# Optimization experiments

Measured on AMD Instinct MI355X. Metric: run time of the kernel, lower is better.

## Reference

```python
import jax, jax.numpy as jnp
import numpy as np

# Module hyperparameters (from init_kwargs)
P = 96                 # num_of_patches
W = 1536.0             # input width
H = 1536.0             # input height
XPS = W / P            # x patch size = 16
YPS = H / P            # y patch size = 16
PROB_THR = 0.9
IOU_THR = 0.5
N = P * P              # total candidate boxes


def setup_inputs() -> dict:
    key = jax.random.key(0)
    # x: [5, P, P] -> channel 0 = probability, 1..4 = (x, y, w, h) in [0,1)
    x = jax.random.uniform(key, (5, P, P), dtype=jnp.float32)
    return {"x": x}


def _pairwise_iou(b):
    # b: [N, 4] xyxy
    x1, y1, x2, y2 = b[:, 0], b[:, 1], b[:, 2], b[:, 3]
    area = (x2 - x1) * (y2 - y1)                       # [N]
    ix1 = jnp.maximum(x1[:, None], x1[None, :])
    iy1 = jnp.maximum(y1[:, None], y1[None, :])
    ix2 = jnp.minimum(x2[:, None], x2[None, :])
    iy2 = jnp.minimum(y2[:, None], y2[None, :])
    inter = jnp.clip(ix2 - ix1, 0.0) * jnp.clip(iy2 - iy1, 0.0)
    union = area[:, None] + area[None, :] - inter
    return jnp.where(union > 0, inter / union, 0.0)    # [N, N]


def _forward(x):
    # --- scale_batch_bbx_xywh, applied densely (invalid entries are masked later) ---
    p = x[0]
    ii = jnp.arange(P, dtype=x.dtype)[:, None]   # row index i
    jj = jnp.arange(P, dtype=x.dtype)[None, :]   # col index j
    bx = x[1] * XPS + ii * XPS
    by = x[2] * YPS + jj * YPS
    bw = x[3] * W
    bh = x[4] * H
    bbx = jnp.stack([p, bx, by, bw, bh], axis=0).reshape(5, N).T   # [N, 5] (p, x, y, w, h)

    # --- remove_low_probability_bbx: fixed-shape validity mask instead of filtering ---
    scores = bbx[:, 0]
    valid = scores > PROB_THR

    # --- convert_batch_to_xyxy + round ---
    x1 = jnp.round(bbx[:, 1])
    y1 = jnp.round(bbx[:, 2])
    x2 = jnp.round(bbx[:, 3] + bbx[:, 1])
    y2 = jnp.round(bbx[:, 4] + bbx[:, 2])

    # --- greedy NMS (torchvision semantics): sort by score desc, suppress by IoU ---
    sort_key = jnp.where(valid, scores, -jnp.inf)
    order = jnp.argsort(-sort_key)
    boxes = jnp.stack([x1, y1, x2, y2], axis=1)[order]   # [N, 4] sorted
    sc = scores[order]
    v = valid[order]
    iou = _pairwise_iou(boxes)                           # [N, N]

    def body(kept, i):
        suppressed = jnp.any(kept & (iou[i] > IOU_THR))
        ki = v[i] & ~suppressed
        return kept.at[i].set(ki), ki

    _, keeps = jax.lax.scan(body, jnp.zeros((N,), bool), jnp.arange(N))

    # --- cat([scores, bbx]) then convert_batch_to_xywh on kept rows ---
    out = jnp.stack(
        [sc, boxes[:, 0], boxes[:, 1], boxes[:, 2] - boxes[:, 0], boxes[:, 3] - boxes[:, 1]],
        axis=1,
    )  # [N, 5] = (score, x, y, w, h), score-descending order like nms output
    out = jnp.where(keeps[:, None], out, 0.0)
    return out, keeps


def reference(x):
    # Returns (out [N,5], keep_mask [N]); rows with keep_mask=False are zeroed.
    # This is the fixed-shape equivalent of the variable-length torch output.
    return _forward(x)
```

## Files before the change

### kernel.cpp

```cpp
#include <hip/hip_runtime.h>

#define PP 96
#define NB (PP*PP)
#define NCH (NB/64)
#define PROB_THR 0.9f
#define FAST_CAP 1024
#define LSTRIDE 1034

typedef unsigned long long u64;
typedef unsigned int u32;

__device__ __forceinline__ void decode_core(int n, float xv, float yv, float wv, float hv,
                                            float& X1, float& Y1, float& X2, float& Y2)
{
    int i = n / PP;
    int j = n - i * PP;
    float bx = __fadd_rn(__fmul_rn(xv, 16.0f), (float)i * 16.0f);
    float by = __fadd_rn(__fmul_rn(yv, 16.0f), (float)j * 16.0f);
    float bw = __fmul_rn(wv, 1536.0f);
    float bh = __fmul_rn(hv, 1536.0f);
    X1 = rintf(bx);
    Y1 = rintf(by);
    X2 = rintf(__fadd_rn(bw, bx));
    Y2 = rintf(__fadd_rn(bh, by));
}

__device__ __forceinline__ void decode_box(const float* __restrict__ x, int n,
                                           float& X1, float& Y1, float& X2, float& Y2)
{
    decode_core(n, x[NB + n], x[2 * NB + n], x[3 * NB + n], x[4 * NB + n], X1, Y1, X2, Y2);
}

__device__ __forceinline__ int iou_hit_nodiv(float ix1, float iy1, float ix2, float iy2, float iar,
                                             float jx1, float jy1, float jx2, float jy2, float jar)
{
    float xx1 = fmaxf(ix1, jx1), yy1 = fmaxf(iy1, jy1);
    float xx2 = fminf(ix2, jx2), yy2 = fminf(iy2, jy2);
    float iw = fmaxf(__fsub_rn(xx2, xx1), 0.0f);
    float ih = fmaxf(__fsub_rn(yy2, yy1), 0.0f);
    float inter = __fmul_rn(iw, ih);
    float uni = __fsub_rn(__fadd_rn(iar, jar), inter);
    return (uni > 0.0f && __fadd_rn(inter, inter) > uni) ? 1 : 0;
}

__device__ __forceinline__ int iou_hit_div(float ix1, float iy1, float ix2, float iy2, float iar,
                                           float jx1, float jy1, float jx2, float jy2, float jar)
{
    float xx1 = fmaxf(ix1, jx1), yy1 = fmaxf(iy1, jy1);
    float xx2 = fminf(ix2, jx2), yy2 = fminf(iy2, jy2);
    float iw = fmaxf(__fsub_rn(xx2, xx1), 0.0f);
    float ih = fmaxf(__fsub_rn(yy2, yy1), 0.0f);
    float inter = __fmul_rn(iw, ih);
    float uni = __fsub_rn(__fadd_rn(iar, jar), inter);
    return (uni > 0.0f && __fdiv_rn(inter, uni) > 0.5f) ? 1 : 0;
}

__global__ void __launch_bounds__(256) k_sort(
    const float* __restrict__ x,
    float* __restrict__ gss, float4* __restrict__ gbox,
    u64* __restrict__ skeys, int* __restrict__ counter, int ws_ok)
{
    __shared__ u64 lmask[NCH];
    __shared__ int pc[NCH], loff[NCH];
    __shared__ int sM;
    __shared__ u64 kdb[FAST_CAP];
    __shared__ int prank[256];

    const int tid = threadIdx.x;
    const int lane = tid & 63;
    const int wv = tid >> 6;
    const int b = blockIdx.x;

    #pragma unroll
    for (int g = 0; g < 36; g += 6) {
        float sv[6];
        #pragma unroll
        for (int u = 0; u < 6; ++u)
            sv[u] = x[((wv * 36 + g + u) << 6) + lane];
        #pragma unroll
        for (int u = 0; u < 6; ++u) {
            u64 m = __ballot(sv[u] > PROB_THR);
            if (lane == 0) lmask[wv * 36 + g + u] = m;
        }
    }
    __syncthreads();
    if (tid < NCH) pc[tid] = __popcll(lmask[tid]);
    __syncthreads();
    if (tid < 64) {
        int acc = 0;
        for (int seg = 0; seg < 3; ++seg) {
            int c = (seg << 6) + lane;
            int pv = (c < NCH) ? pc[c] : 0;
            int v = pv;
            #pragma unroll
            for (int off = 1; off < 64; off <<= 1) {
                int u = __shfl_up(v, off);
                if (lane >= off) v += u;
            }
            if (c < NCH) loff[c] = acc + v - pv;
            acc += __shfl(v, 63);
        }
        if (lane == 0) sM = acc;
    }
    __syncthreads();
    const int M = sM;
    const bool fast = (M <= FAST_CAP) && ws_ok;
    if (b == 0 && tid == 0) counter[0] = M;

    if (!fast) {
        if (b == 0) {
            for (int c = wv; c < NCH; c += 4) {
                float s = x[(c << 6) + lane];
                u64 m = lmask[c];
                if ((m >> lane) & 1ull) {
                    int pos = loff[c] + __popcll(m & ((1ull << lane) - 1ull));
                    int n = (c << 6) + lane;
                    skeys[pos] = ((u64)__float_as_uint(s) << 32) | (u64)(NB - 1 - n);
                }
            }
        }
        return;
    }

    for (int c = wv; c < NCH; c += 4) {
        float s = x[(c << 6) + lane];
        u64 m = lmask[c];
        if ((m >> lane) & 1ull) {
            int pos = loff[c] + __popcll(m & ((1ull << lane) - 1ull));
            int n = (c << 6) + lane;
            kdb[pos] = ((u64)__float_as_uint(s) << 32) | (u64)(NB - 1 - n);
        }
    }
    for (int q = M + tid; q < FAST_CAP; q += 256) kdb[q] = 0ull;
    __syncthreads();

    const int cand = (b << 6) + lane;
    const u64 k0 = kdb[cand];
    const int n0 = NB - 1 - (int)(k0 & 0xFFFFFFFFull);
    float xv0 = x[NB + n0], yv0 = x[2 * NB + n0];
    float wv0 = x[3 * NB + n0], hv0 = x[4 * NB + n0];
    int r = 0;
    const int nck = (M + 63) >> 6;
    for (int ch = wv; ch < nck; ch += 4) {
        u64 kq = kdb[(ch << 6) + lane];
        u32 qlo = (u32)kq, qhi = (u32)(kq >> 32);
        #pragma unroll
        for (int i = 0; i < 64; ++i) {
            u32 blo = (u32)__builtin_amdgcn_readlane((int)qlo, i);
            u32 bhi = (u32)__builtin_amdgcn_readlane((int)qhi, i);
            u64 kb = ((u64)bhi << 32) | (u64)blo;
            r += (kb > k0) ? 1 : 0;
        }
    }
    prank[tid] = r;
    __syncthreads();
    if (tid < 64 && cand < M) {
        int rk = prank[tid] + prank[64 + tid] + prank[128 + tid] + prank[192 + tid];
        float X1, Y1, X2, Y2;
        decode_core(n0, xv0, yv0, wv0, hv0, X1, Y1, X2, Y2);
        gbox[rk] = make_float4(X1, Y1, X2, Y2);
        gss[rk] = __uint_as_float((u32)(k0 >> 32));
    }
}

__global__ void __launch_bounds__(256) k_adj(
    float* __restrict__ out, const float4* __restrict__ gbox,
    const int* __restrict__ counter, u64* __restrict__ adjT, int ws_ok)
{
    __shared__ float4 lb[FAST_CAP];
    __shared__ float la[FAST_CAP];
    int M = counter[0]; if (M > NB) M = NB;
    const int tid = threadIdx.x, lane = tid & 63, wv = tid >> 6, b = blockIdx.x;

    float4 z4 = make_float4(0.f, 0.f, 0.f, 0.f);
    for (int q = tid; q < 216; q += 256)
        ((float4*)out)[b * 216 + q] = z4;

    const bool fast = (M <= FAST_CAP) && ws_ok;
    if (!fast) return;
    if ((b << 4) >= M) return;

    const int W = (M + 63) >> 6;
    for (int f = tid; f < M; f += 256) {
        float4 bb = gbox[f];
        lb[f] = bb;
        la[f] = __fmul_rn(__fsub_rn(bb.z, bb.x), __fsub_rn(bb.w, bb.y));
    }
    __syncthreads();

    #pragma unroll
    for (int r = 0; r < 4; ++r) {
        int i = (b << 4) + (r << 2) + wv;
        if (i >= M) break;
        float4 bi = lb[i];
        float iar = la[i];
        for (int kk = 0; kk < W; ++kk) {
            int j = (kk << 6) + lane;
            float4 bj = lb[j & (FAST_CAP - 1)];
            float jar = la[j & (FAST_CAP - 1)];
            int hit = (j < M) && iou_hit_nodiv(bi.x, bi.y, bi.z, bi.w, iar,
                                               bj.x, bj.y, bj.z, bj.w, jar);
            u64 mm = __ballot(hit);
            if (lane == 0) adjT[((size_t)kk << 10) + i] = mm;
        }
    }
}

__global__ void __launch_bounds__(256) k_sweep(
    const float* __restrict__ x, float* __restrict__ out,
    float* __restrict__ gss, float4* __restrict__ gbox,
    const u64* __restrict__ skeys, const int* __restrict__ counter,
    const u64* __restrict__ adjT, int ws_ok)
{
    __shared__ __align__(16) u64 Lds[16 * LSTRIDE];
    __shared__ u64 keepw[NCH];
    int M = counter[0]; if (M > NB) M = NB;
    const int W = (M + 63) >> 6;
    const bool fast = (M <= FAST_CAP) && ws_ok;
    const int tid = threadIdx.x, lane = tid & 63;

    if (fast) {
        const int npair = W << 9;
        const ulonglong2* gp = (const ulonglong2*)adjT;
        for (int r = 0; r < 4; ++r) {
            int fb = (r << 11) + tid;
            ulonglong2 v[8];
            #pragma unroll
            for (int u = 0; u < 8; ++u) {
                int f = fb + (u << 8);
                v[u] = (f < npair) ? gp[f] : make_ulonglong2(0ull, 0ull);
            }
            #pragma unroll
            for (int u = 0; u < 8; ++u) {
                int f = fb + (u << 8);
                if (f < npair) {
                    int w = f >> 9, r2 = f & 511;
                    ((ulonglong2*)Lds)[w * (LSTRIDE >> 1) + r2] = v[u];
                }
            }
        }
        __syncthreads();

        if (tid < 64) {
            const int wl = (lane < W) ? lane : 0;
            u32 supl = 0u, suph = 0u, dl = 0u, dh = 0u;
            u64 mykw = 0ull;
            const int nrb = (M + 31) >> 5;
            for (int rb = 0; rb < nrb; ++rb) {
                const int c = rb >> 1;
                const int base = rb << 5;
                const ulonglong2* crow = (const ulonglong2*)(Lds + (size_t)c * LSTRIDE + base);
                const ulonglong2* rrow = (const ulonglong2*)(Lds + (size_t)wl * LSTRIDE + base);
                u64 colb[32], rowb[32];
                #pragma unroll
                for (int q = 0; q < 16; ++q) {
                    ulonglong2 t2 = crow[q];
                    colb[2 * q] = t2.x; colb[2 * q + 1] = t2.y;
                }
                #pragma unroll
                for (int q = 0; q < 16; ++q) {
                    ulonglong2 t2 = rrow[q];
                    rowb[2 * q] = t2.x; rowb[2 * q + 1] = t2.y;
                }
                if (!(rb & 1)) {
                    if (rb == 0) { dl = 0u; dh = 0u; }
                    else { dl = (u32)__shfl((int)supl, c); dh = (u32)__shfl((int)suph, c); }
                    int rem = M - (c << 6);
                    if (rem < 64) {
                        if (rem >= 32) dh |= 0xFFFFFFFFu << (rem - 32);
                        else { dh = 0xFFFFFFFFu; dl |= 0xFFFFFFFFu << rem; }
                    }
                }
                u32 kw = 0u;
                if (!(rb & 1)) {
                    #pragma unroll
                    for (int t = 0; t < 32; ++t) {
                        u32 bbit = (dl >> t) & 1u;
                        u32 m = bbit - 1u;
                        dl |= (u32)colb[t] & m;
                        dh |= (u32)(colb[t] >> 32) & m;
                        kw |= m & (1u << t);
                    }
                } else {
                    #pragma unroll
                    for (int t = 0; t < 32; ++t) {
                        u32 bbit = (dh >> t) & 1u;
                        u32 m = bbit - 1u;
                        dl |= (u32)colb[t] & m;
                        dh |= (u32)(colb[t] >> 32) & m;
                        kw |= m & (1u << t);
                    }
                }
                #pragma unroll
                for (int t = 0; t < 32; ++t) {
                    u32 m = 0u - ((kw >> t) & 1u);
                    supl |= (u32)rowb[t] & m;
                    suph |= (u32)(rowb[t] >> 32) & m;
                }
                mykw |= (lane == c) ? ((u64)kw << ((rb & 1) << 5)) : 0ull;
            }
            keepw[lane] = mykw;
        }
    } else {
        for (int t = tid; t < M; t += 256) {
            u64 key = skeys[t];
            int r = 0;
            for (int q = 0; q < M; ++q) r += (skeys[q] > key) ? 1 : 0;
            int n = NB - 1 - (int)(key & 0xFFFFFFFFull);
            float X1, Y1, X2, Y2;
            decode_box(x, n, X1, Y1, X2, Y2);
            gbox[r] = make_float4(X1, Y1, X2, Y2);
            gss[r] = __uint_as_float((u32)(key >> 32));
        }
        __threadfence();
        __syncthreads();
        if (tid < 64) {
            u64 kbs[3] = {0ull, 0ull, 0ull};
            for (int i = 0; i < M; ++i) {
                float4 bi = gbox[i];
                float iar = __fmul_rn(__fsub_rn(bi.z, bi.x), __fsub_rn(bi.w, bi.y));
                int hit = 0;
                int nk = (i > lane) ? ((i - lane + 63) >> 6) : 0;
                for (int w = 0; w < 3 && !hit; ++w) {
                    int klim = nk - (w << 6);
                    if (klim <= 0) break;
                    u64 bits = kbs[w];
                    if (klim < 64) bits &= ((1ull << klim) - 1ull);
                    while (bits) {
                        int kk2 = __builtin_ctzll(bits);
                        bits &= bits - 1ull;
                        int jj = lane + (((w << 6) + kk2) << 6);
                        float4 bj = gbox[jj];
                        float jar = __fmul_rn(__fsub_rn(bj.z, bj.x), __fsub_rn(bj.w, bj.y));
                        if (iou_hit_div(bi.x, bi.y, bi.z, bi.w, iar,
                                        bj.x, bj.y, bj.z, bj.w, jar)) { hit = 1; break; }
                    }
                }
                int suppressed = __any(hit);
                if (!suppressed && lane == (i & 63)) kbs[(i >> 6) >> 6] |= 1ull << ((i >> 6) & 63);
            }
            int NWrd = (M + 63) >> 6;
            for (int wd = 0; wd < NWrd; ++wd) {
                u64 bit = (kbs[wd >> 6] >> (wd & 63)) & 1ull;
                u64 word = __ballot(bit != 0);
                if (lane == 0 && wd < NCH) keepw[wd] = word;
            }
        }
    }
    __syncthreads();

    for (int i = tid; i < M; i += 256) {
        if ((keepw[i >> 6] >> (i & 63)) & 1ull) {
            float4 bb = gbox[i];
            out[i * 5 + 0] = gss[i];
            out[i * 5 + 1] = bb.x;
            out[i * 5 + 2] = bb.y;
            out[i * 5 + 3] = __fsub_rn(bb.z, bb.x);
            out[i * 5 + 4] = __fsub_rn(bb.w, bb.y);
            out[5 * NB + i] = 1.0f;
        }
    }
}

extern "C" void kernel_launch(void* const* d_in, const int* in_sizes, int n_in,
                              void* d_out, int out_size, void* d_ws, size_t ws_size,
                              hipStream_t stream) {
    const float* x = (const float*)d_in[0];
    float* out = (float*)d_out;

    char* ws = (char*)d_ws;
    int* counter = (int*)ws;
    float*  gss  = (float*)(ws + 16);
    float4* gbox = (float4*)(ws + 16 + (size_t)4 * NB);
    u64*    adjT = (u64*)(ws + 16 + (size_t)4 * NB + (size_t)16 * NB);
    u64*    skeys = (u64*)((char*)adjT + (size_t)16384 * 8);
    const size_t NEEDED = 16 + (size_t)4 * NB + (size_t)16 * NB
                        + (size_t)16384 * 8 + (size_t)8 * NB;
    int ws_ok = (ws_size >= NEEDED) ? 1 : 0;

    k_sort<<<16, 256, 0, stream>>>(x, gss, gbox, skeys, counter, ws_ok);
    k_adj<<<64, 256, 0, stream>>>(out, gbox, counter, adjT, ws_ok);
    k_sweep<<<1, 256, 0, stream>>>(x, out, gss, gbox, skeys, counter, adjT, ws_ok);
}
```

Baseline: 104.2 us.

## Merge adjacency and sweep kernels with atomic completion counter handoff

Fuses the IoU adjacency kernel and the single-block sweep kernel into one launch of 65 blocks. Block 0 spins on a global atomic counter until the 64 adjacency blocks signal completion, then runs the greedy sweep. The output zeroing moves into the sort kernel. This removes one kernel launch boundary. In exchange it relies on block 0 co-residing with the other blocks, which it must to avoid deadlock, and the union of shared memory gives every block the larger sweep footprint, which may reduce occupancy.

```diff
diff --git a/kernel.cpp b/kernel.cpp
--- a/kernel.cpp
+++ b/kernel.cpp
@@ -56,9 +56,10 @@
 }
 
 __global__ void __launch_bounds__(256) k_sort(
-    const float* __restrict__ x,
+    const float* __restrict__ x, float* __restrict__ out,
     float* __restrict__ gss, float4* __restrict__ gbox,
-    u64* __restrict__ skeys, int* __restrict__ counter, int ws_ok)
+    u64* __restrict__ skeys, int* __restrict__ counter,
+    int* __restrict__ done, int ws_ok)
 {
     __shared__ u64 lmask[NCH];
     __shared__ int pc[NCH], loff[NCH];
@@ -70,6 +71,13 @@
     const int lane = tid & 63;
     const int wv = tid >> 6;
     const int b = blockIdx.x;
+
+    {
+        float4 z4 = make_float4(0.f, 0.f, 0.f, 0.f);
+        for (int q = tid; q < 864; q += 256)
+            ((float4*)out)[b * 864 + q] = z4;
+        if (b == 0 && tid == 0) done[0] = 0;
+    }
 
     #pragma unroll
     for (int g = 0; g < 36; g += 6) {
@@ -163,63 +171,68 @@
     }
 }
 
-__global__ void __launch_bounds__(256) k_adj(
-    float* __restrict__ out, const float4* __restrict__ gbox,
-    const int* __restrict__ counter, u64* __restrict__ adjT, int ws_ok)
-{
-    __shared__ float4 lb[FAST_CAP];
-    __shared__ float la[FAST_CAP];
-    int M = counter[0]; if (M > NB) M = NB;
-    const int tid = threadIdx.x, lane = tid & 63, wv = tid >> 6, b = blockIdx.x;
-
-    float4 z4 = make_float4(0.f, 0.f, 0.f, 0.f);
-    for (int q = tid; q < 216; q += 256)
-        ((float4*)out)[b * 216 + q] = z4;
-
-    const bool fast = (M <= FAST_CAP) && ws_ok;
-    if (!fast) return;
-    if ((b << 4) >= M) return;
-
-    const int W = (M + 63) >> 6;
-    for (int f = tid; f < M; f += 256) {
-        float4 bb = gbox[f];
-        lb[f] = bb;
-        la[f] = __fmul_rn(__fsub_rn(bb.z, bb.x), __fsub_rn(bb.w, bb.y));
-    }
-    __syncthreads();
-
-    #pragma unroll
-    for (int r = 0; r < 4; ++r) {
-        int i = (b << 4) + (r << 2) + wv;
-        if (i >= M) break;
-        float4 bi = lb[i];
-        float iar = la[i];
-        for (int kk = 0; kk < W; ++kk) {
-            int j = (kk << 6) + lane;
-            float4 bj = lb[j & (FAST_CAP - 1)];
-            float jar = la[j & (FAST_CAP - 1)];
-            int hit = (j < M) && iou_hit_nodiv(bi.x, bi.y, bi.z, bi.w, iar,
-                                               bj.x, bj.y, bj.z, bj.w, jar);
-            u64 mm = __ballot(hit);
-            if (lane == 0) adjT[((size_t)kk << 10) + i] = mm;
-        }
-    }
-}
-
-__global__ void __launch_bounds__(256) k_sweep(
+__global__ void __launch_bounds__(256) k_adjsweep(
     const float* __restrict__ x, float* __restrict__ out,
     float* __restrict__ gss, float4* __restrict__ gbox,
     const u64* __restrict__ skeys, const int* __restrict__ counter,
-    const u64* __restrict__ adjT, int ws_ok)
-{
-    __shared__ __align__(16) u64 Lds[16 * LSTRIDE];
-    __shared__ u64 keepw[NCH];
+    u64* __restrict__ adjT, int* __restrict__ done, int ws_ok)
+{
+    __shared__ __align__(16) union ShU {
+        struct { float4 lb[FAST_CAP]; float la[FAST_CAP]; } p;
+        struct { u64 Lds[16 * LSTRIDE]; u64 keepw[NCH]; } c;
+    } sh;
+
+    const int tid = threadIdx.x, lane = tid & 63, wv = tid >> 6;
+    const int b = blockIdx.x;
+
     int M = counter[0]; if (M > NB) M = NB;
+    const bool fast = (M <= FAST_CAP) && ws_ok;
     const int W = (M + 63) >> 6;
-    const bool fast = (M <= FAST_CAP) && ws_ok;
-    const int tid = threadIdx.x, lane = tid & 63;
+
+    if (b != 0) {
+        if (!fast) return;
+        const int g = b - 1;
+        if ((g << 4) >= M) {
+            if (tid == 0)
+                __hip_atomic_fetch_add(done, 1, __ATOMIC_RELEASE, __HIP_MEMORY_SCOPE_AGENT);
+            return;
+        }
+        for (int f = tid; f < M; f += 256) {
+            float4 bb = gbox[f];
+            sh.p.lb[f] = bb;
+            sh.p.la[f] = __fmul_rn(__fsub_rn(bb.z, bb.x), __fsub_rn(bb.w, bb.y));
+        }
+        __syncthreads();
+        #pragma unroll
+        for (int r = 0; r < 4; ++r) {
+            int i = (g << 4) + (r << 2) + wv;
+            if (i >= M) break;
+            float4 bi = sh.p.lb[i];
+            float iar = sh.p.la[i];
+            for (int kk = 0; kk < W; ++kk) {
+                int j = (kk << 6) + lane;
+                float4 bj = sh.p.lb[j & (FAST_CAP - 1)];
+                float jar = sh.p.la[j & (FAST_CAP - 1)];
+                int hit = (j < M) && iou_hit_nodiv(bi.x, bi.y, bi.z, bi.w, iar,
+                                                   bj.x, bj.y, bj.z, bj.w, jar);
+                u64 mm = __ballot(hit);
+                if (lane == 0) adjT[((size_t)kk << 10) + i] = mm;
+            }
+        }
+        __syncthreads();
+        if (tid == 0)
+            __hip_atomic_fetch_add(done, 1, __ATOMIC_RELEASE, __HIP_MEMORY_SCOPE_AGENT);
+        return;
+    }
 
     if (fast) {
+        if (tid == 0) {
+            while (__hip_atomic_load(done, __ATOMIC_ACQUIRE,
+                                     __HIP_MEMORY_SCOPE_AGENT) < 64)
+                __builtin_amdgcn_s_sleep(2);
+        }
+        __syncthreads();
+
         const int npair = W << 9;
         const ulonglong2* gp = (const ulonglong2*)adjT;
         for (int r = 0; r < 4; ++r) {
@@ -235,7 +248,7 @@
                 int f = fb + (u << 8);
                 if (f < npair) {
                     int w = f >> 9, r2 = f & 511;
-                    ((ulonglong2*)Lds)[w * (LSTRIDE >> 1) + r2] = v[u];
+                    ((ulonglong2*)sh.c.Lds)[w * (LSTRIDE >> 1) + r2] = v[u];
                 }
             }
         }
@@ -249,8 +262,8 @@
             for (int rb = 0; rb < nrb; ++rb) {
                 const int c = rb >> 1;
                 const int base = rb << 5;
-                const ulonglong2* crow = (const ulonglong2*)(Lds + (size_t)c * LSTRIDE + base);
-                const ulonglong2* rrow = (const ulonglong2*)(Lds + (size_t)wl * LSTRIDE + base);
+                const ulonglong2* crow = (const ulonglong2*)(sh.c.Lds + (size_t)c * LSTRIDE + base);
+                const ulonglong2* rrow = (const ulonglong2*)(sh.c.Lds + (size_t)wl * LSTRIDE + base);
                 u64 colb[32], rowb[32];
                 #pragma unroll
                 for (int q = 0; q < 16; ++q) {
@@ -299,7 +312,7 @@
                 }
                 mykw |= (lane == c) ? ((u64)kw << ((rb & 1) << 5)) : 0ull;
             }
-            keepw[lane] = mykw;
+            sh.c.keepw[lane] = mykw;
         }
     } else {
         for (int t = tid; t < M; t += 256) {
@@ -343,14 +356,14 @@
             for (int wd = 0; wd < NWrd; ++wd) {
                 u64 bit = (kbs[wd >> 6] >> (wd & 63)) & 1ull;
                 u64 word = __ballot(bit != 0);
-                if (lane == 0 && wd < NCH) keepw[wd] = word;
+                if (lane == 0 && wd < NCH) sh.c.keepw[wd] = word;
             }
         }
     }
     __syncthreads();
 
     for (int i = tid; i < M; i += 256) {
-        if ((keepw[i >> 6] >> (i & 63)) & 1ull) {
+        if ((sh.c.keepw[i >> 6] >> (i & 63)) & 1ull) {
             float4 bb = gbox[i];
             out[i * 5 + 0] = gss[i];
             out[i * 5 + 1] = bb.x;
@@ -370,6 +383,7 @@
 
     char* ws = (char*)d_ws;
     int* counter = (int*)ws;
+    int* done    = (int*)(ws + 8);
     float*  gss  = (float*)(ws + 16);
     float4* gbox = (float4*)(ws + 16 + (size_t)4 * NB);
     u64*    adjT = (u64*)(ws + 16 + (size_t)4 * NB + (size_t)16 * NB);
@@ -378,7 +392,6 @@
                         + (size_t)16384 * 8 + (size_t)8 * NB;
     int ws_ok = (ws_size >= NEEDED) ? 1 : 0;
 
-    k_sort<<<16, 256, 0, stream>>>(x, gss, gbox, skeys, counter, ws_ok);
-    k_adj<<<64, 256, 0, stream>>>(out, gbox, counter, adjT, ws_ok);
-    k_sweep<<<1, 256, 0, stream>>>(x, out, gss, gbox, skeys, counter, adjT, ws_ok);
-}
+    k_sort<<<16, 256, 0, stream>>>(x, out, gss, gbox, skeys, counter, done, ws_ok);
+    k_adjsweep<<<65, 256, 0, stream>>>(x, out, gss, gbox, skeys, counter, adjT, done, ws_ok);
+}
```

After: 104.7 us. Within noise of the previous version (+0.5%).
